# Kernel optimization log

Measured on AMD Instinct MI355X. Metric: run time of the kernel, lower is better.

Reference implementation:

```python
import jax, jax.numpy as jnp
import numpy as np

B, N, DIM, H = 4, 2048, 64, 8
SCALE = DIM ** -0.5  # qk_scale defaults to head_dim**-0.5 with head_dim = dim


def setup_inputs() -> dict:
    key = jax.random.key(0)
    k1, k2, k3 = jax.random.split(key, 3)
    x = jax.random.normal(k1, (B, N, DIM), dtype=jnp.float32)
    Wqkv = jax.random.normal(k2, (DIM, 3 * H * DIM), dtype=jnp.float32) * (DIM ** -0.5)
    Wproj = jax.random.normal(k3, (H * DIM, DIM), dtype=jnp.float32) * ((H * DIM) ** -0.5)
    bproj = jnp.zeros((DIM,), dtype=jnp.float32)
    return {"x": x, "Wqkv": Wqkv, "Wproj": Wproj, "bproj": bproj}


def reference(x, Wqkv, Wproj, bproj):
    Bx, Nx, C = x.shape
    # qkv: [B,N,3*H*C] -> [B,N,3,H,C] -> (3,B,H,N,C)
    qkv = (x @ Wqkv).reshape(Bx, Nx, 3, H, C).transpose(2, 0, 3, 1, 4)
    q, k, v = qkv[0], qkv[1], qkv[2]
    # scores: [B,H,N,N]
    attn = jax.nn.softmax(jnp.einsum('bhnc,bhmc->bhnm', q, k) * SCALE, axis=-1)
    out = jnp.einsum('bhnm,bhmc->bhnc', attn, v)  # [B,H,N,C]
    out = out.transpose(0, 2, 1, 3).reshape(Bx, Nx, H * C)  # [B,N,H*C]
    return out @ Wproj + bproj  # [B,N,C]
```

## Files before the change

### kernel.cpp

```cpp
#include <hip/hip_runtime.h>

#define NB 4
#define SEQ 2048
#define CD 64
#define NHEAD 8
#define BHN (NB * NHEAD)
#define ROWS (NB * SEQ)
#define HC 512

#define QSCALE 0.18033688011112042f
#define SHIFT  23.083120654223414f

typedef float f32x4 __attribute__((ext_vector_type(4)));
typedef short s16x8 __attribute__((ext_vector_type(8)));
typedef unsigned short u16;
typedef unsigned int u32;

__device__ __forceinline__ u16 f2bf(float x) {
  union { float f; unsigned u; } v; v.f = x;
  unsigned r = v.u + 0x7FFFu + ((v.u >> 16) & 1u);
  return (u16)(r >> 16);
}

__device__ __forceinline__ float fast_exp2(float x) {
#if __has_builtin(__builtin_amdgcn_exp2f)
  return __builtin_amdgcn_exp2f(x);
#else
  return exp2f(x);
#endif
}

__device__ __forceinline__ u32 bitsf(float x) {
  union { float f; u32 u; } v; v.f = x; return v.u;
}

__device__ __forceinline__ u32 pack_trunc(float a, float b) {
#if __has_builtin(__builtin_amdgcn_perm)
  return __builtin_amdgcn_perm(bitsf(b), bitsf(a), 0x07060302u);
#else
  return (bitsf(a) >> 16) | (bitsf(b) & 0xFFFF0000u);
#endif
}

__device__ __forceinline__ u32 pack_rne(float a, float b) {
  return (u32)f2bf(a) | ((u32)f2bf(b) << 16);
}

__device__ __forceinline__ f32x4 mfma_bf16(s16x8 a, s16x8 b, f32x4 c) {
  return __builtin_amdgcn_mfma_f32_16x16x32_bf16(a, b, c, 0, 0, 0);
}

typedef __attribute__((address_space(1))) const u32* gp1;
typedef __attribute__((address_space(3))) u32* lp3;
__device__ __forceinline__ void dma16(const void* g, void* l) {
  __builtin_amdgcn_global_load_lds((gp1)g, (lp3)l, 16, 0, 0);
}

__global__ void __launch_bounds__(256) qkv_kernel(
    const float* __restrict__ x, const float* __restrict__ Wqkv,
    const float* __restrict__ Wproj, u16* __restrict__ Q, u16* __restrict__ K,
    u16* __restrict__ Vt, u16* __restrict__ WpF) {
  const int t = threadIdx.x;

  if (blockIdx.x == 128) {
    for (int i = blockIdx.y * 256 + t; i < 64 * 512; i += 2048) {
      const int f = i >> 9, ln = (i >> 3) & 63, j = i & 7;
      const int col = (f & 3) * 16 + (ln & 15);
      const int k = (f >> 2) * 32 + (ln >> 4) * 8 + j;
      WpF[i] = f2bf(Wproj[k * 64 + col]);
    }
    return;
  }

  __shared__ __align__(16) u16 xs[64 * 72];
  __shared__ __align__(16) u16 wts[192 * 72];

  const int w = t >> 6, lane = t & 63, quad = lane >> 4, c16 = lane & 15;
  const int rb = blockIdx.x * 64;
  const int c0 = blockIdx.y * 192;

  {
    const int row = t >> 2, cc0 = (t & 3) * 16;
    const float* xp = x + (size_t)(rb + row) * CD + cc0;
    union { u16 u[16]; int4 v[2]; } bx;
#pragma unroll
    for (int j = 0; j < 16; j += 4) {
      float4 xv = *(const float4*)(xp + j);
      bx.u[j] = f2bf(xv.x); bx.u[j + 1] = f2bf(xv.y);
      bx.u[j + 2] = f2bf(xv.z); bx.u[j + 3] = f2bf(xv.w);
    }
    *(int4*)&xs[row * 72 + cc0] = bx.v[0];
    *(int4*)&xs[row * 72 + cc0 + 8] = bx.v[1];
  }
#pragma unroll
  for (int p = 0; p < 12; ++p) {
    const int idx = p * 256 + t;
    const int n = idx % 192, k4 = (idx / 192) * 4;
    const float* wp = Wqkv + (size_t)k4 * 1536 + c0 + n;
    const float w0 = wp[0], w1 = wp[1536], w2 = wp[3072], w3 = wp[4608];
    uint2 pk;
    pk.x = pack_rne(w0, w1);
    pk.y = pack_rne(w2, w3);
    *(uint2*)&wts[n * 72 + k4] = pk;
  }
  __syncthreads();

  s16x8 af[2];
#pragma unroll
  for (int kc = 0; kc < 2; ++kc)
    af[kc] = *(const s16x8*)&xs[(w * 16 + c16) * 72 + kc * 32 + quad * 8];

  const int rw = rb + w * 16;
  const int b = rw >> 11;
  const int nn0 = rw & (SEQ - 1);

#pragma unroll
  for (int nb = 0; nb < 12; ++nb) {
    const int cb = c0 + nb * 16;
    const int three = cb >> 9;
    const int h = (cb >> 6) & 7;
    const int ccb = cb & 63;
    const int bhv = b * NHEAD + h;
    s16x8 bf_[2];
#pragma unroll
    for (int kc = 0; kc < 2; ++kc)
      bf_[kc] = *(const s16x8*)&wts[(nb * 16 + c16) * 72 + kc * 32 + quad * 8];

    if (three == 2) {
      f32x4 acc = (f32x4){0.f, 0.f, 0.f, 0.f};
#pragma unroll
      for (int kc = 0; kc < 2; ++kc) acc = mfma_bf16(af[kc], bf_[kc], acc);
      uint2 pk;
      pk.x = pack_rne(acc[0], acc[1]);
      pk.y = pack_rne(acc[2], acc[3]);
      const size_t off = (size_t)bhv * (SEQ * CD) + (size_t)(nn0 >> 5) * 2048 +
                         (size_t)(ccb + c16) * 32 + (rw & 31) + quad * 4;
      *(uint2*)(Vt + off) = pk;
    } else {
      f32x4 acc = (f32x4){0.f, 0.f, 0.f, 0.f};
#pragma unroll
      for (int kc = 0; kc < 2; ++kc) acc = mfma_bf16(bf_[kc], af[kc], acc);
      u16* dstp = (three == 0) ? Q : K;
      const float scl = (three == 0) ? QSCALE : 1.0f;
      uint2 pk;
      pk.x = pack_rne(acc[0] * scl, acc[1] * scl);
      pk.y = pack_rne(acc[2] * scl, acc[3] * scl);
      *(uint2*)(dstp + ((size_t)bhv * SEQ + nn0 + c16) * CD + ccb + quad * 4) =
          pk;
    }
  }
}

__global__ void __launch_bounds__(128, 2) attn_kernel(
    const u16* __restrict__ Q, const u16* __restrict__ K,
    const u16* __restrict__ Vt, u16* __restrict__ O) {
  __shared__ __align__(16) u16 smem[13312];

  const int t = threadIdx.x;
  const int w = t >> 6, lane = t & 63, quad = lane >> 4, c16 = lane & 15;
  const int bh = blockIdx.y;
  const int q0 = blockIdx.x * 64;
  const int kt0 = w * (SEQ / 2);

  u16* KsW = smem + w * 4096;
  u16* VsW = smem + w * 4096 + 2048;
  u16* Pw  = smem + 8192 + w * 2560;

  const u16* Qb = Q + (size_t)bh * SEQ * CD;
  const u16* Kb = K + (size_t)bh * SEQ * CD;
  const u16* Vb = Vt + (size_t)bh * SEQ * CD;

  s16x8 qfb[4][2];
#pragma unroll
  for (int qb = 0; qb < 4; ++qb)
#pragma unroll
    for (int cc = 0; cc < 2; ++cc)
      qfb[qb][cc] = *(const s16x8*)(Qb + (size_t)(q0 + qb * 16 + c16) * CD +
                                    cc * 32 + quad * 8);

  s16x8 onesf;
  {
    const short one = (c16 == 0) ? (short)0x3F80 : (short)0;
#pragma unroll
    for (int j = 0; j < 8; ++j) onesf[j] = one;
  }

  f32x4 o[4][4], osum[4];
#pragma unroll
  for (int qb = 0; qb < 4; ++qb) {
    osum[qb] = (f32x4){0.f, 0.f, 0.f, 0.f};
#pragma unroll
    for (int cb = 0; cb < 4; ++cb) o[qb][cb] = (f32x4){0.f, 0.f, 0.f, 0.f};
  }

  const int krl = lane >> 3, kcl = (lane & 7) ^ ((lane >> 3) & 7);
  const int vrl = lane >> 2, vcl = (lane & 3) ^ ((lane >> 3) & 3);

  int kOff[2][2], vOff[4];
#pragma unroll
  for (int kb = 0; kb < 2; ++kb)
#pragma unroll
    for (int cc = 0; cc < 2; ++cc)
      kOff[kb][cc] = (kb * 16 + c16) * 64 + (((cc * 4 + quad) ^ (c16 & 7)) * 8);
#pragma unroll
  for (int cb = 0; cb < 4; ++cb)
    vOff[cb] = (cb * 16 + c16) * 32 + ((quad ^ ((c16 >> 1) & 3)) * 8);

#define STAGE_TILE(kt_)                                                        \
  {                                                                            \
    const u16* ksrc = Kb + (size_t)(kt_) * CD;                                 \
    _Pragma("unroll") for (int d = 0; d < 4; ++d)                              \
        dma16(ksrc + (size_t)(d * 8 + krl) * CD + kcl * 8, KsW + d * 512);     \
    const u16* vsrc = Vb + (size_t)((kt_) >> 5) * 2048;                        \
    _Pragma("unroll") for (int d = 0; d < 4; ++d)                              \
        dma16(vsrc + (size_t)(d * 16 + vrl) * 32 + vcl * 8, VsW + d * 512);    \
  }

  STAGE_TILE(kt0)

  for (int it = 0; it < 32; ++it) {
    __builtin_amdgcn_s_waitcnt(0x0F70);

    s16x8 kf[2][2], vf[4];
#pragma unroll
    for (int kb = 0; kb < 2; ++kb)
#pragma unroll
      for (int cc = 0; cc < 2; ++cc)
        kf[kb][cc] = *(const s16x8*)&KsW[kOff[kb][cc]];
#pragma unroll
    for (int cb = 0; cb < 4; ++cb)
      vf[cb] = *(const s16x8*)&VsW[vOff[cb]];

    __builtin_amdgcn_s_waitcnt(0xC07F);
    if (it + 1 < 32) STAGE_TILE(kt0 + (it + 1) * 32)

#pragma unroll
    for (int qb = 0; qb < 4; ++qb) {
      u16* Pq = Pw + qb * 640;
#pragma unroll
      for (int kb = 0; kb < 2; ++kb) {
        f32x4 s = (f32x4){-SHIFT, -SHIFT, -SHIFT, -SHIFT};
        s = mfma_bf16(kf[kb][0], qfb[qb][0], s);
        s = mfma_bf16(kf[kb][1], qfb[qb][1], s);
        uint2 pk;
        pk.x = pack_trunc(fast_exp2(s[0]), fast_exp2(s[1]));
        pk.y = pack_trunc(fast_exp2(s[2]), fast_exp2(s[3]));
        *(uint2*)&Pq[c16 * 40 + kb * 16 + quad * 4] = pk;
      }
      const s16x8 pf = *(const s16x8*)&Pq[c16 * 40 + quad * 8];
#pragma unroll
      for (int cb = 0; cb < 4; ++cb)
        o[qb][cb] = mfma_bf16(pf, vf[cb], o[qb][cb]);
      osum[qb] = mfma_bf16(pf, onesf, osum[qb]);
    }
  }
#undef STAGE_TILE

  float* X  = (float*)smem;
  float* Lx = (float*)(smem + 8192);

  __syncthreads();
  if (w == 1) {
#pragma unroll
    for (int qb = 0; qb < 4; ++qb) {
#pragma unroll
      for (int cb = 0; cb < 4; ++cb)
#pragma unroll
        for (int i = 0; i < 4; ++i)
          X[(qb * 16 + quad * 4 + i) * 64 + cb * 16 + c16] = o[qb][cb][i];
      if (c16 == 0)
#pragma unroll
        for (int i = 0; i < 4; ++i)
          Lx[qb * 16 + quad * 4 + i] = osum[qb][i];
    }
  }
  __syncthreads();
  if (w == 0) {
    const int b = bh >> 3, h = bh & 7;
#pragma unroll
    for (int qb = 0; qb < 4; ++qb) {
#pragma unroll
      for (int i = 0; i < 4; ++i) {
        const float l0 = __shfl(osum[qb][i], lane & 48);
        const int qq = qb * 16 + quad * 4 + i;
        const float inv = 1.0f / (l0 + Lx[qq]);
        const int q = q0 + qq;
        u16* dst = O + ((size_t)(b * SEQ + q)) * HC + h * CD;
#pragma unroll
        for (int cb = 0; cb < 4; ++cb)
          dst[cb * 16 + c16] =
              f2bf((o[qb][cb][i] + X[qq * 64 + cb * 16 + c16]) * inv);
      }
    }
  }
}

__global__ void __launch_bounds__(256) proj_kernel(
    const u16* __restrict__ O, const u16* __restrict__ WpF,
    const float* __restrict__ bias, float* __restrict__ out) {
  __shared__ __align__(16) u16 Ls[16 * 520];
  __shared__ __align__(16) float Cred[4][64][20];
  const int t = threadIdx.x;
  const int w = t >> 6, lane = t & 63, quad = lane >> 4, c16 = lane & 15;
  const int r0 = blockIdx.x * 16;

  s16x8 wf[4][4];
#pragma unroll
  for (int kc = 0; kc < 4; ++kc)
#pragma unroll
    for (int nb = 0; nb < 4; ++nb)
      wf[kc][nb] = *(const s16x8*)(WpF + ((((w * 4 + kc) * 4 + nb) << 9) +
                                          lane * 8));

  {
    const int row = t >> 4, cg = (t & 15) * 8;
#pragma unroll
    for (int p = 0; p < 4; ++p)
      *(int4*)&Ls[row * 520 + p * 128 + cg] =
          *(const int4*)(O + (size_t)(r0 + row) * HC + p * 128 + cg);
  }
  __syncthreads();

  f32x4 acc[4];
#pragma unroll
  for (int nb = 0; nb < 4; ++nb) acc[nb] = (f32x4){0.f, 0.f, 0.f, 0.f};
#pragma unroll
  for (int kc = 0; kc < 4; ++kc) {
    const s16x8 af =
        *(const s16x8*)&Ls[c16 * 520 + w * 128 + kc * 32 + quad * 8];
#pragma unroll
    for (int nb = 0; nb < 4; ++nb)
      acc[nb] = mfma_bf16(af, wf[kc][nb], acc[nb]);
  }

#pragma unroll
  for (int nb = 0; nb < 4; ++nb)
    *(f32x4*)&Cred[w][nb * 16 + c16][quad * 4] = acc[nb];
  __syncthreads();

  const int col = t & 63, rbase = (t >> 6) * 4;
  const float bv = bias[col];
#pragma unroll
  for (int j = 0; j < 4; ++j) {
    const int r = rbase + j;
    out[(size_t)(r0 + r) * CD + col] = Cred[0][col][r] + Cred[1][col][r] +
                                       Cred[2][col][r] + Cred[3][col][r] + bv;
  }
}

extern "C" void kernel_launch(void* const* d_in, const int* in_sizes, int n_in,
                              void* d_out, int out_size, void* d_ws, size_t ws_size,
                              hipStream_t stream) {
  (void)in_sizes; (void)n_in; (void)out_size; (void)ws_size;
  const float* x     = (const float*)d_in[0];
  const float* Wqkv  = (const float*)d_in[1];
  const float* Wproj = (const float*)d_in[2];
  const float* bproj = (const float*)d_in[3];
  float* out = (float*)d_out;

  u16* WpF = (u16*)d_ws;
  u16* Qw  = WpF + CD * HC;
  u16* Kw  = Qw + (size_t)BHN * SEQ * CD;
  u16* Vtw = Kw + (size_t)BHN * SEQ * CD;
  u16* Ow  = Vtw + (size_t)BHN * SEQ * CD;

  qkv_kernel<<<dim3(129, 8), 256, 0, stream>>>(x, Wqkv, Wproj, Qw, Kw, Vtw,
                                               WpF);
  attn_kernel<<<dim3(32, 32), 128, 0, stream>>>(Qw, Kw, Vtw, Ow);
  proj_kernel<<<512, 256, 0, stream>>>(Ow, WpF, bproj, out);
}
```

Before: 123.5 us.

## Fuse output projection into attention kernel via per-head atomic accumulation

```diff
diff --git a/kernel.cpp b/kernel.cpp
--- a/kernel.cpp
+++ b/kernel.cpp
@@ -48,6 +48,10 @@
 
 __device__ __forceinline__ f32x4 mfma_bf16(s16x8 a, s16x8 b, f32x4 c) {
   return __builtin_amdgcn_mfma_f32_16x16x32_bf16(a, b, c, 0, 0, 0);
+}
+
+__device__ __forceinline__ void atomAddF32(float* p, float v) {
+  __hip_atomic_fetch_add(p, v, __ATOMIC_RELAXED, __HIP_MEMORY_SCOPE_AGENT);
 }
 
 typedef __attribute__((address_space(1))) const u32* gp1;
@@ -151,9 +155,10 @@
   }
 }
 
-__global__ void __launch_bounds__(128, 2) attn_kernel(
+__global__ void __launch_bounds__(128, 2) attnproj_kernel(
     const u16* __restrict__ Q, const u16* __restrict__ K,
-    const u16* __restrict__ Vt, u16* __restrict__ O) {
+    const u16* __restrict__ Vt, const u16* __restrict__ WpF,
+    const float* __restrict__ bias, float* __restrict__ out) {
   __shared__ __align__(16) u16 smem[13312];
 
   const int t = threadIdx.x;
@@ -256,95 +261,83 @@
   }
 #undef STAGE_TILE
 
-  float* X  = (float*)smem;
-  float* Lx = (float*)(smem + 8192);
+  float* Xo = (float*)smem;
+  float* Lo = (float*)(smem + 8192);
+  u16*  Ot  = smem + 8320;
 
   __syncthreads();
-  if (w == 1) {
-#pragma unroll
-    for (int qb = 0; qb < 4; ++qb) {
+#pragma unroll
+  for (int j = 0; j < 2; ++j) {
+    const int qb = (w ^ 1) * 2 + j;
+#pragma unroll
+    for (int cb = 0; cb < 4; ++cb)
+#pragma unroll
+      for (int i = 0; i < 4; ++i)
+        Xo[(w ^ 1) * 2048 + (j * 16 + quad * 4 + i) * 64 + cb * 16 + c16] =
+            o[qb][cb][i];
+    if (c16 == 0)
+#pragma unroll
+      for (int i = 0; i < 4; ++i)
+        Lo[(w ^ 1) * 32 + j * 16 + quad * 4 + i] = osum[qb][i];
+  }
+  __syncthreads();
+#pragma unroll
+  for (int j = 0; j < 2; ++j) {
+    const int qb = w * 2 + j;
+#pragma unroll
+    for (int i = 0; i < 4; ++i) {
+      const float l =
+          __shfl(osum[qb][i], lane & 48) + Lo[w * 32 + j * 16 + quad * 4 + i];
+      const float inv = 1.0f / l;
+      const int qq = qb * 16 + quad * 4 + i;
 #pragma unroll
       for (int cb = 0; cb < 4; ++cb)
-#pragma unroll
-        for (int i = 0; i < 4; ++i)
-          X[(qb * 16 + quad * 4 + i) * 64 + cb * 16 + c16] = o[qb][cb][i];
-      if (c16 == 0)
-#pragma unroll
-        for (int i = 0; i < 4; ++i)
-          Lx[qb * 16 + quad * 4 + i] = osum[qb][i];
+        Ot[qq * 72 + cb * 16 + c16] = f2bf(
+            (o[qb][cb][i] +
+             Xo[w * 2048 + (j * 16 + quad * 4 + i) * 64 + cb * 16 + c16]) *
+            inv);
     }
   }
   __syncthreads();
-  if (w == 0) {
-    const int b = bh >> 3, h = bh & 7;
-#pragma unroll
-    for (int qb = 0; qb < 4; ++qb) {
-#pragma unroll
-      for (int i = 0; i < 4; ++i) {
-        const float l0 = __shfl(osum[qb][i], lane & 48);
-        const int qq = qb * 16 + quad * 4 + i;
-        const float inv = 1.0f / (l0 + Lx[qq]);
-        const int q = q0 + qq;
-        u16* dst = O + ((size_t)(b * SEQ + q)) * HC + h * CD;
-#pragma unroll
-        for (int cb = 0; cb < 4; ++cb)
-          dst[cb * 16 + c16] =
-              f2bf((o[qb][cb][i] + X[qq * 64 + cb * 16 + c16]) * inv);
-      }
-    }
-  }
-}
-
-__global__ void __launch_bounds__(256) proj_kernel(
-    const u16* __restrict__ O, const u16* __restrict__ WpF,
-    const float* __restrict__ bias, float* __restrict__ out) {
-  __shared__ __align__(16) u16 Ls[16 * 520];
-  __shared__ __align__(16) float Cred[4][64][20];
-  const int t = threadIdx.x;
-  const int w = t >> 6, lane = t & 63, quad = lane >> 4, c16 = lane & 15;
-  const int r0 = blockIdx.x * 16;
-
-  s16x8 wf[4][4];
-#pragma unroll
-  for (int kc = 0; kc < 4; ++kc)
-#pragma unroll
-    for (int nb = 0; nb < 4; ++nb)
-      wf[kc][nb] = *(const s16x8*)(WpF + ((((w * 4 + kc) * 4 + nb) << 9) +
-                                          lane * 8));
-
-  {
-    const int row = t >> 4, cg = (t & 15) * 8;
-#pragma unroll
-    for (int p = 0; p < 4; ++p)
-      *(int4*)&Ls[row * 520 + p * 128 + cg] =
-          *(const int4*)(O + (size_t)(r0 + row) * HC + p * 128 + cg);
-  }
-  __syncthreads();
-
-  f32x4 acc[4];
-#pragma unroll
-  for (int nb = 0; nb < 4; ++nb) acc[nb] = (f32x4){0.f, 0.f, 0.f, 0.f};
-#pragma unroll
-  for (int kc = 0; kc < 4; ++kc) {
-    const s16x8 af =
-        *(const s16x8*)&Ls[c16 * 520 + w * 128 + kc * 32 + quad * 8];
-#pragma unroll
-    for (int nb = 0; nb < 4; ++nb)
-      acc[nb] = mfma_bf16(af, wf[kc][nb], acc[nb]);
-  }
-
-#pragma unroll
-  for (int nb = 0; nb < 4; ++nb)
-    *(f32x4*)&Cred[w][nb * 16 + c16][quad * 4] = acc[nb];
-  __syncthreads();
-
-  const int col = t & 63, rbase = (t >> 6) * 4;
-  const float bv = bias[col];
-#pragma unroll
-  for (int j = 0; j < 4; ++j) {
-    const int r = rbase + j;
-    out[(size_t)(r0 + r) * CD + col] = Cred[0][col][r] + Cred[1][col][r] +
-                                       Cred[2][col][r] + Cred[3][col][r] + bv;
+
+  const int b = bh >> 3, h = bh & 7;
+  s16x8 aF[2][2];
+#pragma unroll
+  for (int j = 0; j < 2; ++j)
+#pragma unroll
+    for (int cc = 0; cc < 2; ++cc)
+      aF[j][cc] =
+          *(const s16x8*)&Ot[((w * 2 + j) * 16 + c16) * 72 + cc * 32 + quad * 8];
+
+  f32x4 c_[2][4];
+#pragma unroll
+  for (int j = 0; j < 2; ++j)
+#pragma unroll
+    for (int nb = 0; nb < 4; ++nb) c_[j][nb] = (f32x4){0.f, 0.f, 0.f, 0.f};
+
+#pragma unroll
+  for (int cc = 0; cc < 2; ++cc)
+#pragma unroll
+    for (int nb = 0; nb < 4; ++nb) {
+      const s16x8 wfv =
+          *(const s16x8*)(WpF + ((((h * 2 + cc) * 4 + nb) << 9) + lane * 8));
+#pragma unroll
+      for (int j = 0; j < 2; ++j)
+        c_[j][nb] = mfma_bf16(aF[j][cc], wfv, c_[j][nb]);
+    }
+
+#pragma unroll
+  for (int nb = 0; nb < 4; ++nb) {
+    const int col = nb * 16 + c16;
+    const float badd = (h == 0) ? bias[col] : 0.0f;
+#pragma unroll
+    for (int j = 0; j < 2; ++j) {
+      const int qbase = q0 + (w * 2 + j) * 16 + quad * 4;
+#pragma unroll
+      for (int i = 0; i < 4; ++i)
+        atomAddF32(out + (size_t)(b * SEQ + qbase + i) * CD + col,
+                   c_[j][nb][i] + badd);
+    }
   }
 }
 
@@ -362,10 +355,10 @@
   u16* Qw  = WpF + CD * HC;
   u16* Kw  = Qw + (size_t)BHN * SEQ * CD;
   u16* Vtw = Kw + (size_t)BHN * SEQ * CD;
-  u16* Ow  = Vtw + (size_t)BHN * SEQ * CD;
 
   qkv_kernel<<<dim3(129, 8), 256, 0, stream>>>(x, Wqkv, Wproj, Qw, Kw, Vtw,
                                                WpF);
-  attn_kernel<<<dim3(32, 32), 128, 0, stream>>>(Qw, Kw, Vtw, Ow);
-  proj_kernel<<<512, 256, 0, stream>>>(Ow, WpF, bproj, out);
-}
+  hipMemsetAsync(out, 0, (size_t)ROWS * CD * sizeof(float), stream);
+  attnproj_kernel<<<dim3(32, 32), 128, 0, stream>>>(Qw, Kw, Vtw, WpF, bproj,
+                                                    out);
+}
```

Measured after the change: 141.6 us. 14.7% more time.

## Store K/V in MFMA fragment order and load directly to registers

Applied to the files above, without the earlier changes.

```diff
diff --git a/kernel.cpp b/kernel.cpp
--- a/kernel.cpp
+++ b/kernel.cpp
@@ -50,16 +50,11 @@
   return __builtin_amdgcn_mfma_f32_16x16x32_bf16(a, b, c, 0, 0, 0);
 }
 
-typedef __attribute__((address_space(1))) const u32* gp1;
-typedef __attribute__((address_space(3))) u32* lp3;
-__device__ __forceinline__ void dma16(const void* g, void* l) {
-  __builtin_amdgcn_global_load_lds((gp1)g, (lp3)l, 16, 0, 0);
-}
 
 __global__ void __launch_bounds__(256) qkv_kernel(
     const float* __restrict__ x, const float* __restrict__ Wqkv,
-    const float* __restrict__ Wproj, u16* __restrict__ Q, u16* __restrict__ K,
-    u16* __restrict__ Vt, u16* __restrict__ WpF) {
+    const float* __restrict__ Wproj, u16* __restrict__ Q, u16* __restrict__ Kf,
+    u16* __restrict__ Vf, u16* __restrict__ WpF) {
   const int t = threadIdx.x;
 
   if (blockIdx.x == 128) {
@@ -133,42 +128,56 @@
       uint2 pk;
       pk.x = pack_rne(acc[0], acc[1]);
       pk.y = pack_rne(acc[2], acc[3]);
-      const size_t off = (size_t)bhv * (SEQ * CD) + (size_t)(nn0 >> 5) * 2048 +
-                         (size_t)(ccb + c16) * 32 + (rw & 31) + quad * 4;
-      *(uint2*)(Vt + off) = pk;
+      const int tile = nn0 >> 5;
+      const int cb_ = ccb >> 4;
+      const int kq = (nn0 & 31) + quad * 4;
+      const size_t off = (size_t)bhv * (SEQ * CD) + (size_t)tile * 2048 +
+                         cb_ * 512 + (kq >> 3) * 128 + c16 * 8 + (kq & 4);
+      *(uint2*)(Vf + off) = pk;
+    } else if (three == 1) {
+      f32x4 acc = (f32x4){0.f, 0.f, 0.f, 0.f};
+#pragma unroll
+      for (int kc = 0; kc < 2; ++kc) acc = mfma_bf16(bf_[kc], af[kc], acc);
+      uint2 pk;
+      pk.x = pack_rne(acc[0], acc[1]);
+      pk.y = pack_rne(acc[2], acc[3]);
+      const int tile = nn0 >> 5;
+      const int kb_ = (nn0 >> 4) & 1;
+      const int cc_ = ccb >> 5;
+      const int cq = (ccb & 31) + quad * 4;
+      const size_t off = (size_t)bhv * (SEQ * CD) + (size_t)tile * 2048 +
+                         (kb_ * 2 + cc_) * 512 + (cq >> 3) * 128 + c16 * 8 +
+                         (cq & 4);
+      *(uint2*)(Kf + off) = pk;
     } else {
       f32x4 acc = (f32x4){0.f, 0.f, 0.f, 0.f};
 #pragma unroll
       for (int kc = 0; kc < 2; ++kc) acc = mfma_bf16(bf_[kc], af[kc], acc);
-      u16* dstp = (three == 0) ? Q : K;
-      const float scl = (three == 0) ? QSCALE : 1.0f;
       uint2 pk;
-      pk.x = pack_rne(acc[0] * scl, acc[1] * scl);
-      pk.y = pack_rne(acc[2] * scl, acc[3] * scl);
-      *(uint2*)(dstp + ((size_t)bhv * SEQ + nn0 + c16) * CD + ccb + quad * 4) =
-          pk;
+      pk.x = pack_rne(acc[0] * QSCALE, acc[1] * QSCALE);
+      pk.y = pack_rne(acc[2] * QSCALE, acc[3] * QSCALE);
+      *(uint2*)(Q + ((size_t)bhv * SEQ + nn0 + c16) * CD + ccb + quad * 4) = pk;
     }
   }
 }
 
 __global__ void __launch_bounds__(128, 2) attn_kernel(
-    const u16* __restrict__ Q, const u16* __restrict__ K,
-    const u16* __restrict__ Vt, u16* __restrict__ O) {
-  __shared__ __align__(16) u16 smem[13312];
+    const u16* __restrict__ Q, const u16* __restrict__ Kf,
+    const u16* __restrict__ Vf, u16* __restrict__ O) {
+  __shared__ __align__(16) u16 smem[8320];
 
   const int t = threadIdx.x;
   const int w = t >> 6, lane = t & 63, quad = lane >> 4, c16 = lane & 15;
   const int bh = blockIdx.y;
   const int q0 = blockIdx.x * 64;
-  const int kt0 = w * (SEQ / 2);
-
-  u16* KsW = smem + w * 4096;
-  u16* VsW = smem + w * 4096 + 2048;
-  u16* Pw  = smem + 8192 + w * 2560;
+
+  u16* Pw = smem + w * 2560;
 
   const u16* Qb = Q + (size_t)bh * SEQ * CD;
-  const u16* Kb = K + (size_t)bh * SEQ * CD;
-  const u16* Vb = Vt + (size_t)bh * SEQ * CD;
+  const u16* KbT = Kf + (size_t)bh * (SEQ * CD) + (size_t)w * 32 * 2048 +
+                   lane * 8;
+  const u16* VbT = Vf + (size_t)bh * (SEQ * CD) + (size_t)w * 32 * 2048 +
+                   lane * 8;
 
   s16x8 qfb[4][2];
 #pragma unroll
@@ -193,68 +202,45 @@
     for (int cb = 0; cb < 4; ++cb) o[qb][cb] = (f32x4){0.f, 0.f, 0.f, 0.f};
   }
 
-  const int krl = lane >> 3, kcl = (lane & 7) ^ ((lane >> 3) & 7);
-  const int vrl = lane >> 2, vcl = (lane & 3) ^ ((lane >> 3) & 3);
-
-  int kOff[2][2], vOff[4];
-#pragma unroll
-  for (int kb = 0; kb < 2; ++kb)
-#pragma unroll
-    for (int cc = 0; cc < 2; ++cc)
-      kOff[kb][cc] = (kb * 16 + c16) * 64 + (((cc * 4 + quad) ^ (c16 & 7)) * 8);
-#pragma unroll
-  for (int cb = 0; cb < 4; ++cb)
-    vOff[cb] = (cb * 16 + c16) * 32 + ((quad ^ ((c16 >> 1) & 3)) * 8);
-
-#define STAGE_TILE(kt_)                                                        \
+  s16x8 ka[4], va[4], kb2[4], vb2[4];
+
+#define LOAD_TILE(kf_, vf_, it_)                                               \
   {                                                                            \
-    const u16* ksrc = Kb + (size_t)(kt_) * CD;                                 \
-    _Pragma("unroll") for (int d = 0; d < 4; ++d)                              \
-        dma16(ksrc + (size_t)(d * 8 + krl) * CD + kcl * 8, KsW + d * 512);     \
-    const u16* vsrc = Vb + (size_t)((kt_) >> 5) * 2048;                        \
-    _Pragma("unroll") for (int d = 0; d < 4; ++d)                              \
-        dma16(vsrc + (size_t)(d * 16 + vrl) * 32 + vcl * 8, VsW + d * 512);    \
-  }
-
-  STAGE_TILE(kt0)
-
-  for (int it = 0; it < 32; ++it) {
-    __builtin_amdgcn_s_waitcnt(0x0F70);
-
-    s16x8 kf[2][2], vf[4];
-#pragma unroll
-    for (int kb = 0; kb < 2; ++kb)
-#pragma unroll
-      for (int cc = 0; cc < 2; ++cc)
-        kf[kb][cc] = *(const s16x8*)&KsW[kOff[kb][cc]];
-#pragma unroll
-    for (int cb = 0; cb < 4; ++cb)
-      vf[cb] = *(const s16x8*)&VsW[vOff[cb]];
-
-    __builtin_amdgcn_s_waitcnt(0xC07F);
-    if (it + 1 < 32) STAGE_TILE(kt0 + (it + 1) * 32)
-
-#pragma unroll
-    for (int qb = 0; qb < 4; ++qb) {
-      u16* Pq = Pw + qb * 640;
-#pragma unroll
-      for (int kb = 0; kb < 2; ++kb) {
-        f32x4 s = (f32x4){-SHIFT, -SHIFT, -SHIFT, -SHIFT};
-        s = mfma_bf16(kf[kb][0], qfb[qb][0], s);
-        s = mfma_bf16(kf[kb][1], qfb[qb][1], s);
-        uint2 pk;
-        pk.x = pack_trunc(fast_exp2(s[0]), fast_exp2(s[1]));
-        pk.y = pack_trunc(fast_exp2(s[2]), fast_exp2(s[3]));
-        *(uint2*)&Pq[c16 * 40 + kb * 16 + quad * 4] = pk;
-      }
-      const s16x8 pf = *(const s16x8*)&Pq[c16 * 40 + quad * 8];
-#pragma unroll
-      for (int cb = 0; cb < 4; ++cb)
-        o[qb][cb] = mfma_bf16(pf, vf[cb], o[qb][cb]);
-      osum[qb] = mfma_bf16(pf, onesf, osum[qb]);
-    }
-  }
-#undef STAGE_TILE
+    _Pragma("unroll") for (int fi = 0; fi < 4; ++fi)                           \
+        kf_[fi] = *(const s16x8*)(KbT + (it_) * 2048 + fi * 512);              \
+    _Pragma("unroll") for (int cb = 0; cb < 4; ++cb)                           \
+        vf_[cb] = *(const s16x8*)(VbT + (it_) * 2048 + cb * 512);              \
+  }
+
+#define COMPUTE_TILE(kf_, vf_)                                                 \
+  {                                                                            \
+    _Pragma("unroll") for (int qb = 0; qb < 4; ++qb) {                         \
+      u16* Pq = Pw + qb * 640;                                                 \
+      _Pragma("unroll") for (int kb = 0; kb < 2; ++kb) {                       \
+        f32x4 s = (f32x4){-SHIFT, -SHIFT, -SHIFT, -SHIFT};                     \
+        s = mfma_bf16(kf_[kb * 2], qfb[qb][0], s);                             \
+        s = mfma_bf16(kf_[kb * 2 + 1], qfb[qb][1], s);                         \
+        uint2 pk;                                                              \
+        pk.x = pack_trunc(fast_exp2(s[0]), fast_exp2(s[1]));                   \
+        pk.y = pack_trunc(fast_exp2(s[2]), fast_exp2(s[3]));                   \
+        *(uint2*)&Pq[c16 * 40 + kb * 16 + quad * 4] = pk;                      \
+      }                                                                        \
+      const s16x8 pf = *(const s16x8*)&Pq[c16 * 40 + quad * 8];                \
+      _Pragma("unroll") for (int cb = 0; cb < 4; ++cb)                         \
+          o[qb][cb] = mfma_bf16(pf, vf_[cb], o[qb][cb]);                       \
+      osum[qb] = mfma_bf16(pf, onesf, osum[qb]);                               \
+    }                                                                          \
+  }
+
+  LOAD_TILE(ka, va, 0)
+  for (int it = 0; it < 32; it += 2) {
+    if (it + 1 < 32) LOAD_TILE(kb2, vb2, it + 1)
+    COMPUTE_TILE(ka, va)
+    if (it + 2 < 32) LOAD_TILE(ka, va, it + 2)
+    if (it + 1 < 32) COMPUTE_TILE(kb2, vb2)
+  }
+#undef LOAD_TILE
+#undef COMPUTE_TILE
 
   float* X  = (float*)smem;
   float* Lx = (float*)(smem + 8192);
@@ -360,12 +346,12 @@
 
   u16* WpF = (u16*)d_ws;
   u16* Qw  = WpF + CD * HC;
-  u16* Kw  = Qw + (size_t)BHN * SEQ * CD;
-  u16* Vtw = Kw + (size_t)BHN * SEQ * CD;
-  u16* Ow  = Vtw + (size_t)BHN * SEQ * CD;
-
-  qkv_kernel<<<dim3(129, 8), 256, 0, stream>>>(x, Wqkv, Wproj, Qw, Kw, Vtw,
+  u16* Kfw = Qw + (size_t)BHN * SEQ * CD;
+  u16* Vfw = Kfw + (size_t)BHN * SEQ * CD;
+  u16* Ow  = Vfw + (size_t)BHN * SEQ * CD;
+
+  qkv_kernel<<<dim3(129, 8), 256, 0, stream>>>(x, Wqkv, Wproj, Qw, Kfw, Vfw,
                                                WpF);
-  attn_kernel<<<dim3(32, 32), 128, 0, stream>>>(Qw, Kw, Vtw, Ow);
+  attn_kernel<<<dim3(32, 32), 128, 0, stream>>>(Qw, Kfw, Vfw, Ow);
   proj_kernel<<<512, 256, 0, stream>>>(Ow, WpF, bproj, out);
 }
```

Result: faster. 120.8 us (-2.2%).
